# Optimization experiments

Measured on AMD Instinct MI355X. Metric: run time of the kernel, lower is better.

The kernel has to match this reference:

```python
import jax, jax.numpy as jnp
import numpy as np

EPS = 1e-12

def _l1_normalize(x, axis=1):
    # torch.nn.functional.normalize(p=1): x / max(||x||_1, eps)
    n = jnp.sum(jnp.abs(x), axis=axis, keepdims=True)
    return x / jnp.maximum(n, EPS)

def setup_inputs() -> dict:
    key = jax.random.key(0)
    k1, k2 = jax.random.split(key)
    B, M, C = 8192, 16, 345
    y_pred = jax.random.normal(k1, (B, 1, M * C), dtype=jnp.float32)
    labels = jax.random.randint(k2, (B,), 0, C, dtype=jnp.int64)
    return {"y_pred": y_pred, "labels": labels, "class_type": C, "model_num": M, "num_local": 4}

def reference(y_pred, labels, class_type, model_num, num_local):
    B = y_pred.shape[0]
    M, C = model_num, class_type
    logits = y_pred.reshape(B, M, C)  # y_pred.squeeze(1), split into per-model blocks
    rows = jnp.arange(B)

    # per-model softmax over classes (softmax_multi_child_pred)
    probs = jax.nn.softmax(logits, axis=-1)  # [B, M, C]
    # gather per-sample true-class prob for each model: probs[i, :, labels[i]] -> [B, M]
    true_p = probs[rows, :, labels]
    true_confs = jax.lax.stop_gradient(jax.nn.softmax(true_p, axis=1))  # detached

    # use_true_conf=True -> weights = true_confs
    weights = true_confs

    # num_local < model_num: topk select + scatter + L1 normalize (post_weights)
    vals, idx = jax.lax.top_k(weights, num_local)  # [B, k]
    post = jnp.zeros_like(weights).at[rows[:, None], idx].set(vals)
    post_weights = _l1_normalize(post, axis=1)

    weighted_mat = _l1_normalize(weights, axis=1)

    # strided weighted ensemble sum: sum_m y_pred[:, i::C] * w  ==  einsum over models
    ems_out = jnp.einsum('bmc,bm->bc', logits, weighted_mat)
    ems_out_post = jnp.einsum('bmc,bm->bc', logits, post_weights)

    # per-model, per-sample cross entropy (reduction='none')
    logp = jax.nn.log_softmax(logits, axis=-1)
    each_point_loss = -logp[rows, :, labels]  # [B, M]

    # BCEWithLogitsLoss(softmax(weighted_mat), softmax(true_confs))
    x = jax.nn.softmax(weighted_mat, axis=-1)
    t = jax.nn.softmax(true_confs, axis=-1)
    confidence_loss = jnp.mean(jnp.maximum(x, 0.0) - x * t + jnp.log1p(jnp.exp(-jnp.abs(x))))

    wm_soft = jax.nn.softmax(weighted_mat, axis=-1)
    child_loss = jnp.mean(each_point_loss * wm_soft)

    ensemble_loss = jnp.mean(-jax.nn.log_softmax(ems_out, axis=-1)[rows, labels])

    return (ems_out_post, child_loss, confidence_loss, ensemble_loss, wm_soft, true_confs)
```

## Files before the change

kernel.cpp:

```cpp
#include <hip/hip_runtime.h>
#include <math.h>

#define MM 16
#define CC 345
#define MC (MM*CC)
#define KTOP 4
#define GAP_THR 3e-7f
#define NT 256

__device__ __forceinline__ float fexp(float x) { return __expf(x); }
__device__ __forceinline__ float flog(float x) { return __logf(x); }

__device__ __forceinline__ float rmax16(float v) {
    #pragma unroll
    for (int off = 8; off; off >>= 1) v = fmaxf(v, __shfl_xor(v, off, 16));
    return v;
}
__device__ __forceinline__ float rmin16(float v) {
    #pragma unroll
    for (int off = 8; off; off >>= 1) v = fminf(v, __shfl_xor(v, off, 16));
    return v;
}
__device__ __forceinline__ float rsum16(float v) {
    #pragma unroll
    for (int off = 8; off; off >>= 1) v += __shfl_xor(v, off, 16);
    return v;
}

__global__ __launch_bounds__(NT)
void ens_main(const float* __restrict__ y, const int* __restrict__ labels,
              float* __restrict__ out, float* __restrict__ partial, int B)
{
    const int b   = blockIdx.x;
    const int tid = threadIdx.x;

    __shared__ float sl[MC + 64];
    __shared__ float s_truep[MM], s_epl[MM], s_mx[MM], s_tpp[MM];
    __shared__ float s_w[MM], s_pw[MM];
    __shared__ float s_red[NT/64];
    __shared__ float s_lab;
    __shared__ int   s_need;
    __shared__ unsigned s_selmask;

    const int label = labels[b];
    const float* yb = y + (size_t)b * MC;

    {
        const int w  = tid >> 6;
        const int lw = tid & 63;
        const float4* src = reinterpret_cast<const float4*>(yb) + w * 345;
        float4* dst = reinterpret_cast<float4*>(sl) + w * 345;
        for (int i = lw; i < 345; i += 64) dst[i] = src[i];

        const int m = tid >> 4;
        const int l = tid & 15;
        const float* row = sl + m * CC;
        float v[22];
        float mx = -INFINITY;
        #pragma unroll
        for (int k = 0; k < 22; ++k) {
            const int c = l + (k << 4);
            if (c < CC) { v[k] = row[c]; mx = fmaxf(mx, v[k]); }
            else          v[k] = 0.f;
        }
        mx = rmax16(mx);
        float se = 0.f;
        #pragma unroll
        for (int k = 0; k < 22; ++k) {
            const int c = l + (k << 4);
            if (c < CC) se += fexp(v[k] - mx);
        }
        se = rsum16(se);
        if (l == 0) {
            const float lt = row[label];
            s_mx[m]    = mx;
            s_truep[m] = fexp(lt - mx) / se;
            s_epl[m]   = -(lt - mx - flog(se));
        }
    }
    __syncthreads();

    if (tid < MM) {
        const int l = tid;
        const size_t off_wm = (size_t)B * CC + 3;
        const size_t off_tc = off_wm + (size_t)B * MM;

        const float tp = s_truep[l];
        const float mx = rmax16(tp);
        const float e  = fexp(tp - mx);
        const float tc = e / rsum16(e);
        const float s1 = fmaxf(rsum16(fabsf(tc)), 1e-12f);
        const float wm = tc / s1;
        int rank = 0;
        #pragma unroll
        for (int j = 0; j < MM; ++j) {
            const float vj = __shfl(tc, j, 16);
            rank += (vj > tc) || (vj == tc && j < l);
        }
        const bool sel = (rank < KTOP);
        const float val4 = rmin16(sel ? tc : INFINITY);
        const float val5 = rmax16(sel ? -INFINITY : tc);
        if (l == 0) s_need = (val4 - val5 < GAP_THR) ? 1 : 0;

        const float post = sel ? tc : 0.f;
        const float psum = fmaxf(rsum16(fabsf(post)), 1e-12f);
        s_pw[l] = post / psum;
        s_w[l]  = wm;

        const float mw = rmax16(wm);
        const float ex = fexp(wm - mw);
        const float xv = ex / rsum16(ex);
        const float mt = rmax16(tc);
        const float et = fexp(tc - mt);
        const float tv = et / rsum16(et);
        const float childp = s_epl[l] * xv;
        const float confp  = fmaxf(xv, 0.f) - xv * tv + flog(1.f + fexp(-fabsf(xv)));
        const float childs = rsum16(childp);
        const float confs  = rsum16(confp);
        if (l == 0) {
            partial[(size_t)b * 3 + 0] = childs;
            partial[(size_t)b * 3 + 1] = confs;
        }
        out[off_wm + (size_t)b * MM + l] = xv;
        out[off_tc + (size_t)b * MM + l] = tc;
    }
    __syncthreads();

    if (s_need) {
        {
            const int m = tid >> 4;
            const int l = tid & 15;
            const float* row = sl + m * CC;
            const float mx = s_mx[m];
            float se = 0.f;
            for (int c = l; c < CC; c += 16) se += expf(row[c] - mx);
            se = rsum16(se);
            if (l == 0) s_tpp[m] = expf(row[label] - mx) / se;
        }
        __syncthreads();
        if (tid == 0) {
            float tcp[MM];
            float mxx = -INFINITY;
            for (int m = 0; m < MM; ++m) mxx = fmaxf(mxx, s_tpp[m]);
            float ses = 0.f;
            for (int m = 0; m < MM; ++m) { tcp[m] = expf(s_tpp[m] - mxx); ses += tcp[m]; }
            for (int m = 0; m < MM; ++m) tcp[m] /= ses;
            bool used[MM];
            for (int m = 0; m < MM; ++m) used[m] = false;
            unsigned msk = 0;
            for (int k = 0; k < KTOP; ++k) {
                int bi = -1; float bv = -INFINITY;
                for (int m = 0; m < MM; ++m)
                    if (!used[m] && tcp[m] > bv) { bv = tcp[m]; bi = m; }
                used[bi] = true; msk |= (1u << bi);
            }
            s_selmask = msk;
        }
        __syncthreads();
        if (tid < MM) {
            const int l = tid;
            const float tp = s_truep[l];
            const float mx = rmax16(tp);
            const float e  = fexp(tp - mx);
            const float tc = e / rsum16(e);
            const bool sel2 = ((s_selmask >> l) & 1u) != 0;
            const float post = sel2 ? tc : 0.f;
            const float psum = fmaxf(rsum16(fabsf(post)), 1e-12f);
            s_pw[l] = post / psum;
        }
        __syncthreads();
    }

    {
        const int c0 = tid;
        const int c1 = tid + NT;
        const bool act1 = (c1 < CC);
        float a0 = 0.f, p0 = 0.f, a1 = 0.f, p1 = 0.f;
        #pragma unroll
        for (int m = 0; m < MM; ++m) {
            const float w_ = s_w[m];
            const float q_ = s_pw[m];
            const float v0 = sl[m * CC + c0];
            a0 = fmaf(v0, w_, a0);
            p0 = fmaf(v0, q_, p0);
            if (act1) {
                const float v1 = sl[m * CC + c1];
                a1 = fmaf(v1, w_, a1);
                p1 = fmaf(v1, q_, p1);
            }
        }
        if (c0 == label) s_lab = a0;
        if (act1 && c1 == label) s_lab = a1;
        out[(size_t)b * CC + c0] = p0;
        if (act1) out[(size_t)b * CC + c1] = p1;

        float e = fexp(a0) + (act1 ? fexp(a1) : 0.f);
        #pragma unroll
        for (int off = 32; off; off >>= 1) e += __shfl_xor(e, off);
        if ((tid & 63) == 0) s_red[tid >> 6] = e;
        __syncthreads();
        if (tid == 0) {
            float s = 0.f;
            #pragma unroll
            for (int w = 0; w < NT/64; ++w) s += s_red[w];
            partial[(size_t)b * 3 + 2] = -(s_lab - flog(s));
        }
    }
}

__global__ __launch_bounds__(64)
void ens_reduce1(const float* __restrict__ partial, double* __restrict__ ws2, int B)
{
    const int t  = threadIdx.x;
    const int i  = blockIdx.x;
    const int r0 = i * 128 + t * 2;
    double c = 0.0, f = 0.0, e = 0.0;
    #pragma unroll
    for (int k = 0; k < 2; ++k) {
        const int r = r0 + k;
        c += (double)partial[(size_t)r * 3 + 0];
        f += (double)partial[(size_t)r * 3 + 1];
        e += (double)partial[(size_t)r * 3 + 2];
    }
    #pragma unroll
    for (int off = 32; off; off >>= 1) {
        c += __shfl_xor(c, off);
        f += __shfl_xor(f, off);
        e += __shfl_xor(e, off);
    }
    if (t == 0) {
        ws2[(size_t)i * 3 + 0] = c;
        ws2[(size_t)i * 3 + 1] = f;
        ws2[(size_t)i * 3 + 2] = e;
    }
}

__global__ __launch_bounds__(64)
void ens_reduce2(const double* __restrict__ ws2, float* __restrict__ out, int B)
{
    const int t = threadIdx.x;
    double c = ws2[(size_t)t * 3 + 0];
    double f = ws2[(size_t)t * 3 + 1];
    double e = ws2[(size_t)t * 3 + 2];
    #pragma unroll
    for (int off = 32; off; off >>= 1) {
        c += __shfl_xor(c, off);
        f += __shfl_xor(f, off);
        e += __shfl_xor(e, off);
    }
    if (t == 0) {
        const size_t base = (size_t)B * CC;
        out[base + 0] = (float)(c / (double)((size_t)B * MM));
        out[base + 1] = (float)(f / (double)((size_t)B * MM));
        out[base + 2] = (float)(e / (double)B);
    }
}

extern "C" void kernel_launch(void* const* d_in, const int* in_sizes, int n_in,
                              void* d_out, int out_size, void* d_ws, size_t ws_size,
                              hipStream_t stream)
{
    const float* y      = (const float*)d_in[0];
    const int*   labels = (const int*)d_in[1];
    const int    B      = in_sizes[1];
    float* out     = (float*)d_out;
    float* partial = (float*)d_ws;
    double* ws2    = (double*)((char*)d_ws + (((size_t)B * 3 * sizeof(float) + 255) & ~(size_t)255));

    ens_main<<<dim3(B), dim3(NT), 0, stream>>>(y, labels, out, partial, B);
    ens_reduce1<<<dim3(64), dim3(64), 0, stream>>>(partial, ws2, B);
    ens_reduce2<<<dim3(1), dim3(64), 0, stream>>>(ws2, out, B);
}
```

Before: 55.96 us.

## Make main kernel persistent and prefetch next sample's logits into registers

The main kernel becomes a grid-stride persistent kernel with a fixed grid of 1792 blocks instead of one block per sample. While the weighted ensemble sums for the current sample are computed, each warp loads the next sample's logit block into registers, then copies it to shared memory at the end of the iteration. This is meant to overlap the global load latency with compute and cut per-block launch overhead. The trade-offs are higher register pressure from the float4 prefetch buffer, a launch-bounds occupancy hint, and tail imbalance because the batch does not divide evenly by the grid.

```diff
diff --git a/kernel.cpp b/kernel.cpp
--- a/kernel.cpp
+++ b/kernel.cpp
@@ -7,6 +7,7 @@
 #define KTOP 4
 #define GAP_THR 3e-7f
 #define NT 256
+#define GRID 1792
 
 __device__ __forceinline__ float fexp(float x) { return __expf(x); }
 __device__ __forceinline__ float flog(float x) { return __logf(x); }
@@ -27,12 +28,13 @@
     return v;
 }
 
-__global__ __launch_bounds__(NT)
+__global__ __launch_bounds__(NT, 8)
 void ens_main(const float* __restrict__ y, const int* __restrict__ labels,
               float* __restrict__ out, float* __restrict__ partial, int B)
 {
-    const int b   = blockIdx.x;
     const int tid = threadIdx.x;
+    const int w   = tid >> 6;
+    const int lw  = tid & 63;
 
     __shared__ float sl[MC + 64];
     __shared__ float s_truep[MM], s_epl[MM], s_mx[MM], s_tpp[MM];
@@ -42,168 +44,192 @@
     __shared__ int   s_need;
     __shared__ unsigned s_selmask;
 
-    const int label = labels[b];
-    const float* yb = y + (size_t)b * MC;
-
-    {
-        const int w  = tid >> 6;
-        const int lw = tid & 63;
-        const float4* src = reinterpret_cast<const float4*>(yb) + w * 345;
+    int b = blockIdx.x;
+    if (b < B) {
+        const float4* src = reinterpret_cast<const float4*>(y + (size_t)b * MC) + w * 345;
         float4* dst = reinterpret_cast<float4*>(sl) + w * 345;
         for (int i = lw; i < 345; i += 64) dst[i] = src[i];
-
-        const int m = tid >> 4;
-        const int l = tid & 15;
-        const float* row = sl + m * CC;
-        float v[22];
-        float mx = -INFINITY;
-        #pragma unroll
-        for (int k = 0; k < 22; ++k) {
-            const int c = l + (k << 4);
-            if (c < CC) { v[k] = row[c]; mx = fmaxf(mx, v[k]); }
-            else          v[k] = 0.f;
-        }
-        mx = rmax16(mx);
-        float se = 0.f;
-        #pragma unroll
-        for (int k = 0; k < 22; ++k) {
-            const int c = l + (k << 4);
-            if (c < CC) se += fexp(v[k] - mx);
-        }
-        se = rsum16(se);
-        if (l == 0) {
-            const float lt = row[label];
-            s_mx[m]    = mx;
-            s_truep[m] = fexp(lt - mx) / se;
-            s_epl[m]   = -(lt - mx - flog(se));
-        }
-    }
-    __syncthreads();
-
-    if (tid < MM) {
-        const int l = tid;
-        const size_t off_wm = (size_t)B * CC + 3;
-        const size_t off_tc = off_wm + (size_t)B * MM;
-
-        const float tp = s_truep[l];
-        const float mx = rmax16(tp);
-        const float e  = fexp(tp - mx);
-        const float tc = e / rsum16(e);
-        const float s1 = fmaxf(rsum16(fabsf(tc)), 1e-12f);
-        const float wm = tc / s1;
-        int rank = 0;
-        #pragma unroll
-        for (int j = 0; j < MM; ++j) {
-            const float vj = __shfl(tc, j, 16);
-            rank += (vj > tc) || (vj == tc && j < l);
-        }
-        const bool sel = (rank < KTOP);
-        const float val4 = rmin16(sel ? tc : INFINITY);
-        const float val5 = rmax16(sel ? -INFINITY : tc);
-        if (l == 0) s_need = (val4 - val5 < GAP_THR) ? 1 : 0;
-
-        const float post = sel ? tc : 0.f;
-        const float psum = fmaxf(rsum16(fabsf(post)), 1e-12f);
-        s_pw[l] = post / psum;
-        s_w[l]  = wm;
-
-        const float mw = rmax16(wm);
-        const float ex = fexp(wm - mw);
-        const float xv = ex / rsum16(ex);
-        const float mt = rmax16(tc);
-        const float et = fexp(tc - mt);
-        const float tv = et / rsum16(et);
-        const float childp = s_epl[l] * xv;
-        const float confp  = fmaxf(xv, 0.f) - xv * tv + flog(1.f + fexp(-fabsf(xv)));
-        const float childs = rsum16(childp);
-        const float confs  = rsum16(confp);
-        if (l == 0) {
-            partial[(size_t)b * 3 + 0] = childs;
-            partial[(size_t)b * 3 + 1] = confs;
-        }
-        out[off_wm + (size_t)b * MM + l] = xv;
-        out[off_tc + (size_t)b * MM + l] = tc;
-    }
-    __syncthreads();
-
-    if (s_need) {
+    }
+
+    for (; b < B; b += GRID) {
+        const int label = labels[b];
+        const int bn = b + GRID;
+        const bool havenext = (bn < B);
+
         {
             const int m = tid >> 4;
             const int l = tid & 15;
             const float* row = sl + m * CC;
-            const float mx = s_mx[m];
+            float v[22];
+            float mx = -INFINITY;
+            #pragma unroll
+            for (int k = 0; k < 22; ++k) {
+                const int c = l + (k << 4);
+                if (c < CC) { v[k] = row[c]; mx = fmaxf(mx, v[k]); }
+                else          v[k] = 0.f;
+            }
+            mx = rmax16(mx);
             float se = 0.f;
-            for (int c = l; c < CC; c += 16) se += expf(row[c] - mx);
+            #pragma unroll
+            for (int k = 0; k < 22; ++k) {
+                const int c = l + (k << 4);
+                if (c < CC) se += fexp(v[k] - mx);
+            }
             se = rsum16(se);
-            if (l == 0) s_tpp[m] = expf(row[label] - mx) / se;
+            if (l == 0) {
+                const float lt = row[label];
+                s_mx[m]    = mx;
+                s_truep[m] = fexp(lt - mx) / se;
+                s_epl[m]   = -(lt - mx - flog(se));
+            }
         }
         __syncthreads();
-        if (tid == 0) {
-            float tcp[MM];
-            float mxx = -INFINITY;
-            for (int m = 0; m < MM; ++m) mxx = fmaxf(mxx, s_tpp[m]);
-            float ses = 0.f;
-            for (int m = 0; m < MM; ++m) { tcp[m] = expf(s_tpp[m] - mxx); ses += tcp[m]; }
-            for (int m = 0; m < MM; ++m) tcp[m] /= ses;
-            bool used[MM];
-            for (int m = 0; m < MM; ++m) used[m] = false;
-            unsigned msk = 0;
-            for (int k = 0; k < KTOP; ++k) {
-                int bi = -1; float bv = -INFINITY;
-                for (int m = 0; m < MM; ++m)
-                    if (!used[m] && tcp[m] > bv) { bv = tcp[m]; bi = m; }
-                used[bi] = true; msk |= (1u << bi);
-            }
-            s_selmask = msk;
-        }
-        __syncthreads();
+
         if (tid < MM) {
             const int l = tid;
+            const size_t off_wm = (size_t)B * CC + 3;
+            const size_t off_tc = off_wm + (size_t)B * MM;
+
             const float tp = s_truep[l];
             const float mx = rmax16(tp);
             const float e  = fexp(tp - mx);
             const float tc = e / rsum16(e);
-            const bool sel2 = ((s_selmask >> l) & 1u) != 0;
-            const float post = sel2 ? tc : 0.f;
+            const float s1 = fmaxf(rsum16(fabsf(tc)), 1e-12f);
+            const float wm = tc / s1;
+            int rank = 0;
+            #pragma unroll
+            for (int j = 0; j < MM; ++j) {
+                const float vj = __shfl(tc, j, 16);
+                rank += (vj > tc) || (vj == tc && j < l);
+            }
+            const bool sel = (rank < KTOP);
+            const float val4 = rmin16(sel ? tc : INFINITY);
+            const float val5 = rmax16(sel ? -INFINITY : tc);
+            if (l == 0) s_need = (val4 - val5 < GAP_THR) ? 1 : 0;
+
+            const float post = sel ? tc : 0.f;
             const float psum = fmaxf(rsum16(fabsf(post)), 1e-12f);
             s_pw[l] = post / psum;
+            s_w[l]  = wm;
+
+            const float mw = rmax16(wm);
+            const float ex = fexp(wm - mw);
+            const float xv = ex / rsum16(ex);
+            const float mt = rmax16(tc);
+            const float et = fexp(tc - mt);
+            const float tv = et / rsum16(et);
+            const float childp = s_epl[l] * xv;
+            const float confp  = fmaxf(xv, 0.f) - xv * tv + flog(1.f + fexp(-fabsf(xv)));
+            const float childs = rsum16(childp);
+            const float confs  = rsum16(confp);
+            if (l == 0) {
+                partial[(size_t)b * 3 + 0] = childs;
+                partial[(size_t)b * 3 + 1] = confs;
+            }
+            out[off_wm + (size_t)b * MM + l] = xv;
+            out[off_tc + (size_t)b * MM + l] = tc;
         }
         __syncthreads();
-    }
-
-    {
-        const int c0 = tid;
-        const int c1 = tid + NT;
-        const bool act1 = (c1 < CC);
-        float a0 = 0.f, p0 = 0.f, a1 = 0.f, p1 = 0.f;
-        #pragma unroll
-        for (int m = 0; m < MM; ++m) {
-            const float w_ = s_w[m];
-            const float q_ = s_pw[m];
-            const float v0 = sl[m * CC + c0];
-            a0 = fmaf(v0, w_, a0);
-            p0 = fmaf(v0, q_, p0);
-            if (act1) {
-                const float v1 = sl[m * CC + c1];
-                a1 = fmaf(v1, w_, a1);
-                p1 = fmaf(v1, q_, p1);
-            }
-        }
-        if (c0 == label) s_lab = a0;
-        if (act1 && c1 == label) s_lab = a1;
-        out[(size_t)b * CC + c0] = p0;
-        if (act1) out[(size_t)b * CC + c1] = p1;
-
-        float e = fexp(a0) + (act1 ? fexp(a1) : 0.f);
-        #pragma unroll
-        for (int off = 32; off; off >>= 1) e += __shfl_xor(e, off);
-        if ((tid & 63) == 0) s_red[tid >> 6] = e;
-        __syncthreads();
-        if (tid == 0) {
-            float s = 0.f;
-            #pragma unroll
-            for (int w = 0; w < NT/64; ++w) s += s_red[w];
-            partial[(size_t)b * 3 + 2] = -(s_lab - flog(s));
+
+        if (s_need) {
+            {
+                const int m = tid >> 4;
+                const int l = tid & 15;
+                const float* row = sl + m * CC;
+                const float mx = s_mx[m];
+                float se = 0.f;
+                for (int c = l; c < CC; c += 16) se += expf(row[c] - mx);
+                se = rsum16(se);
+                if (l == 0) s_tpp[m] = expf(row[label] - mx) / se;
+            }
+            __syncthreads();
+            if (tid == 0) {
+                float tcp[MM];
+                float mxx = -INFINITY;
+                for (int m = 0; m < MM; ++m) mxx = fmaxf(mxx, s_tpp[m]);
+                float ses = 0.f;
+                for (int m = 0; m < MM; ++m) { tcp[m] = expf(s_tpp[m] - mxx); ses += tcp[m]; }
+                for (int m = 0; m < MM; ++m) tcp[m] /= ses;
+                bool used[MM];
+                for (int m = 0; m < MM; ++m) used[m] = false;
+                unsigned msk = 0;
+                for (int k = 0; k < KTOP; ++k) {
+                    int bi = -1; float bv = -INFINITY;
+                    for (int m = 0; m < MM; ++m)
+                        if (!used[m] && tcp[m] > bv) { bv = tcp[m]; bi = m; }
+                    used[bi] = true; msk |= (1u << bi);
+                }
+                s_selmask = msk;
+            }
+            __syncthreads();
+            if (tid < MM) {
+                const int l = tid;
+                const float tp = s_truep[l];
+                const float mx = rmax16(tp);
+                const float e  = fexp(tp - mx);
+                const float tc = e / rsum16(e);
+                const bool sel2 = ((s_selmask >> l) & 1u) != 0;
+                const float post = sel2 ? tc : 0.f;
+                const float psum = fmaxf(rsum16(fabsf(post)), 1e-12f);
+                s_pw[l] = post / psum;
+            }
+            __syncthreads();
+        }
+
+        {
+            float4 pf[6];
+            if (havenext) {
+                const float4* srcn =
+                    reinterpret_cast<const float4*>(y + (size_t)bn * MC) + w * 345;
+                #pragma unroll
+                for (int k = 0; k < 6; ++k) {
+                    const int i = lw + (k << 6);
+                    if (i < 345) pf[k] = srcn[i];
+                }
+            }
+
+            const int c0 = tid;
+            const int c1 = tid + NT;
+            const bool act1 = (c1 < CC);
+            float a0 = 0.f, p0 = 0.f, a1 = 0.f, p1 = 0.f;
+            #pragma unroll
+            for (int m = 0; m < MM; ++m) {
+                const float w_ = s_w[m];
+                const float q_ = s_pw[m];
+                const float v0 = sl[m * CC + c0];
+                a0 = fmaf(v0, w_, a0);
+                p0 = fmaf(v0, q_, p0);
+                if (act1) {
+                    const float v1 = sl[m * CC + c1];
+                    a1 = fmaf(v1, w_, a1);
+                    p1 = fmaf(v1, q_, p1);
+                }
+            }
+            if (c0 == label) s_lab = a0;
+            if (act1 && c1 == label) s_lab = a1;
+            out[(size_t)b * CC + c0] = p0;
+            if (act1) out[(size_t)b * CC + c1] = p1;
+
+            float e = fexp(a0) + (act1 ? fexp(a1) : 0.f);
+            #pragma unroll
+            for (int off = 32; off; off >>= 1) e += __shfl_xor(e, off);
+            if ((tid & 63) == 0) s_red[tid >> 6] = e;
+            __syncthreads();
+            if (tid == 0) {
+                float s = 0.f;
+                #pragma unroll
+                for (int q = 0; q < NT/64; ++q) s += s_red[q];
+                partial[(size_t)b * 3 + 2] = -(s_lab - flog(s));
+            }
+
+            if (havenext) {
+                float4* dst = reinterpret_cast<float4*>(sl) + w * 345;
+                #pragma unroll
+                for (int k = 0; k < 6; ++k) {
+                    const int i = lw + (k << 6);
+                    if (i < 345) dst[i] = pf[k];
+                }
+            }
         }
     }
 }
@@ -267,7 +293,7 @@
     float* partial = (float*)d_ws;
     double* ws2    = (double*)((char*)d_ws + (((size_t)B * 3 * sizeof(float) + 255) & ~(size_t)255));
 
-    ens_main<<<dim3(B), dim3(NT), 0, stream>>>(y, labels, out, partial, B);
+    ens_main<<<dim3(GRID), dim3(NT), 0, stream>>>(y, labels, out, partial, B);
     ens_reduce1<<<dim3(64), dim3(64), 0, stream>>>(partial, ws2, B);
     ens_reduce2<<<dim3(1), dim3(64), 0, stream>>>(ws2, out, B);
 }
```

Measured after the change: 88.57 us. 58.3% more time.
